# Optimization experiments

Hardware: AMD Instinct MI355X
Metric: run time of the kernel (lower is better)

## Reference

```python
import jax, jax.numpy as jnp
import numpy as np

REFRACTORY_PERIOD = 5
DAMPENING_FACTOR = 0.3


def setup_inputs() -> dict:
    key = jax.random.key(0)
    B, T, N = 32, 4096, 256
    x = jax.random.normal(key, (B, T, N), dtype=jnp.float32)
    return {"x": x}


def _refractory_scan(x):
    # x: [B, T, N]; scan over time keeping refractory counter q resident.
    B, T, N = x.shape
    xt = jnp.swapaxes(x, 0, 1)  # [T, B, N]

    def step(q, x_t):
        cond = (x_t > 0) & (q == 0)
        z_t = jnp.where(cond, jnp.ones_like(q), jnp.zeros_like(q))
        q = jnp.maximum(jnp.zeros_like(q), q - 1) + REFRACTORY_PERIOD * z_t
        return q, z_t

    q0 = jnp.zeros((B, N), dtype=x.dtype)
    # Note: the t=0 case in the original (z0 = x0>0, q = R*z0) is exactly the
    # first step of this scan starting from q0 = 0.
    _, z = jax.lax.scan(step, q0, xt)
    return jnp.swapaxes(z, 0, 1)  # [B, T, N]


def reference(x) -> jnp.ndarray:
    # Forward value is exactly z_forward (the surrogate-gradient straight-through
    # construction leaves the value unchanged).
    return _refractory_scan(x)
```

## Files before the change

kernel.cpp:

```cpp
#include <hip/hip_runtime.h>
#include <cstdint>
#include <cstddef>

#define BB 32
#define TT 4096
#define NNV 64
#define CC 32
#define PSUB 4
#define PG 32
#define NCH 256

__device__ __forceinline__ uint32_t comp6(uint32_t f, uint32_t g) {
    uint32_t h = 0;
    #pragma unroll
    for (int e = 0; e < 6; ++e) {
        const uint32_t fe = (f >> (4 * e)) & 0xFu;
        h |= ((g >> (4 * fe)) & 0xFu) << (4 * e);
    }
    return h;
}

__device__ __forceinline__ uint32_t tbl_from_mask(uint32_t m) {
    uint32_t tbl = 0;
    #pragma unroll
    for (int e = 0; e < 6; ++e) {
        int na = e;
        #pragma unroll
        for (int it = 0; it < 6; ++it) {
            const uint32_t r = (na < 32) ? (m >> na) : 0u;
            const int t = na + (r ? __builtin_ctz(r) : 0);
            na = r ? (t + 6) : na;
        }
        const int q = na > CC ? na - CC : 0;
        tbl |= (uint32_t)q << (4 * e);
    }
    return tbl;
}

__global__ __launch_bounds__(256) void k_scan(const float* __restrict__ x,
                                              uint4* __restrict__ msk,
                                              uint32_t* __restrict__ gtab) {
    const int tid = threadIdx.x;
    const int pg = blockIdx.x >> 5;
    const int b  = blockIdx.x & 31;
    const int psub = tid >> 6;
    const int n4 = tid & 63;
    const int p = pg * PSUB + psub;

    const float4* __restrict__ xv = reinterpret_cast<const float4*>(x)
        + ((size_t)b * TT + (size_t)p * CC) * NNV + n4;

    uint32_t cur[4] = {0u, 0u, 0u, 0u};
    #pragma unroll
    for (int jb = 0; jb < CC; jb += 8) {
        float4 buf[8];
        #pragma unroll
        for (int u = 0; u < 8; ++u)
            buf[u] = xv[(size_t)(jb + u) * NNV];
        #pragma unroll
        for (int u = 0; u < 8; ++u) {
            const int j = jb + u;
            cur[0] |= (buf[u].x > 0.0f) ? (1u << j) : 0u;
            cur[1] |= (buf[u].y > 0.0f) ? (1u << j) : 0u;
            cur[2] |= (buf[u].z > 0.0f) ? (1u << j) : 0u;
            cur[3] |= (buf[u].w > 0.0f) ? (1u << j) : 0u;
        }
    }

    msk[(size_t)blockIdx.x * 256 + tid] = make_uint4(cur[0], cur[1], cur[2], cur[3]);

    __shared__ uint32_t tbl[PSUB][NCH];
    __shared__ uint32_t aux[2][NCH];
    #pragma unroll
    for (int c = 0; c < 4; ++c)
        tbl[psub][n4 * 4 + c] = tbl_from_mask(cur[c]);
    __syncthreads();
    aux[0][tid] = comp6(tbl[0][tid], tbl[1][tid]);
    aux[1][tid] = comp6(tbl[2][tid], tbl[3][tid]);
    __syncthreads();
    gtab[(size_t)blockIdx.x * 256 + tid] = comp6(aux[0][tid], aux[1][tid]);
}

__global__ __launch_bounds__(256) void k_emit(const uint4* __restrict__ msk,
                                              const uint32_t* __restrict__ gtab,
                                              float* __restrict__ z) {
    const int tid = threadIdx.x;
    const int pg = blockIdx.x >> 5;
    const int b  = blockIdx.x & 31;
    const int psub = tid >> 6;
    const int n4 = tid & 63;
    const int p = pg * PSUB + psub;

    __shared__ uint32_t gl[PG - 1][NCH];
    __shared__ uint32_t tbl[PSUB][NCH];
    __shared__ uint8_t  ent[PSUB][NCH];

    for (int i = tid; i < pg * NCH; i += 256)
        gl[0][i] = gtab[((size_t)(i >> 8) * 32 + b) * 256 + (i & 255)];

    const uint4 mv = msk[(size_t)blockIdx.x * 256 + tid];
    uint32_t cur[4] = {mv.x, mv.y, mv.z, mv.w};
    #pragma unroll
    for (int c = 0; c < 4; ++c)
        tbl[psub][n4 * 4 + c] = tbl_from_mask(cur[c]);
    __syncthreads();

    {
        int e = 0;
        for (int g = 0; g < pg; ++g)
            e = (int)((gl[g][tid] >> (4 * e)) & 0xFu);
        #pragma unroll
        for (int s = 0; s < PSUB; ++s) {
            ent[s][tid] = (uint8_t)e;
            e = (int)((tbl[s][tid] >> (4 * e)) & 0xFu);
        }
    }
    __syncthreads();

    float4* __restrict__ zv = reinterpret_cast<float4*>(z)
        + ((size_t)b * TT + (size_t)p * CC) * NNV + n4;

    const uint32_t e4 = reinterpret_cast<const uint32_t*>(ent[psub])[n4];
    uint32_t spk[4];
    #pragma unroll
    for (int c = 0; c < 4; ++c) {
        const uint32_t m = cur[c];
        int na = (int)((e4 >> (8 * c)) & 0xFFu);
        uint32_t s = 0;
        #pragma unroll
        for (int it = 0; it < 6; ++it) {
            const uint32_t r = (na < 32) ? (m >> na) : 0u;
            const int t = na + (r ? __builtin_ctz(r) : 0);
            s |= r ? (1u << (t & 31)) : 0u;
            na = r ? (t + 6) : na;
        }
        spk[c] = s;
    }

    #pragma unroll
    for (int j = 0; j < CC; ++j) {
        float4 o;
        o.x = ((spk[0] >> j) & 1u) ? 1.0f : 0.0f;
        o.y = ((spk[1] >> j) & 1u) ? 1.0f : 0.0f;
        o.z = ((spk[2] >> j) & 1u) ? 1.0f : 0.0f;
        o.w = ((spk[3] >> j) & 1u) ? 1.0f : 0.0f;
        zv[(size_t)j * NNV] = o;
    }
}

extern "C" void kernel_launch(void* const* d_in, const int* in_sizes, int n_in,
                              void* d_out, int out_size, void* d_ws, size_t ws_size,
                              hipStream_t stream) {
    const float* x = (const float*)d_in[0];
    float* z = (float*)d_out;
    uint4* msk = (uint4*)d_ws;
    uint32_t* gtab = (uint32_t*)((char*)d_ws + (size_t)BB * PG * PSUB * NCH * 4);

    k_scan<<<dim3(BB * PG), 256, 0, stream>>>(x, msk, gtab);
    k_emit<<<dim3(BB * PG), 256, 0, stream>>>(msk, gtab, z);
}
```

Measured before the change: 251.4 us.

## Stage scan tables in output buffer, add resolve kernel, use nontemporal stores

```diff
diff --git a/kernel.cpp b/kernel.cpp
--- a/kernel.cpp
+++ b/kernel.cpp
@@ -9,6 +9,16 @@
 #define PSUB 4
 #define PG 32
 #define NCH 256
+#define OFF_MSK 0u
+#define OFF_MAP 4096u
+#define OFF_TBL 5120u
+#define OFF_ENT 9216u
+
+typedef float f32x4 __attribute__((ext_vector_type(4)));
+
+__device__ __forceinline__ char* region_of(float* z, int b, int pg) {
+    return (char*)(z + ((size_t)b * TT + (size_t)pg * (CC * PSUB)) * NCH);
+}
 
 __device__ __forceinline__ uint32_t comp6(uint32_t f, uint32_t g) {
     uint32_t h = 0;
@@ -38,8 +48,7 @@
 }
 
 __global__ __launch_bounds__(256) void k_scan(const float* __restrict__ x,
-                                              uint4* __restrict__ msk,
-                                              uint32_t* __restrict__ gtab) {
+                                              float* __restrict__ z) {
     const int tid = threadIdx.x;
     const int pg = blockIdx.x >> 5;
     const int b  = blockIdx.x & 31;
@@ -67,23 +76,58 @@
         }
     }
 
-    msk[(size_t)blockIdx.x * 256 + tid] = make_uint4(cur[0], cur[1], cur[2], cur[3]);
+    char* regionB = region_of(z, b, pg);
+    reinterpret_cast<uint4*>(regionB + OFF_MSK)[tid] =
+        make_uint4(cur[0], cur[1], cur[2], cur[3]);
 
     __shared__ uint32_t tbl[PSUB][NCH];
     __shared__ uint32_t aux[2][NCH];
+    uint32_t* tblg = reinterpret_cast<uint32_t*>(regionB + OFF_TBL);
     #pragma unroll
-    for (int c = 0; c < 4; ++c)
-        tbl[psub][n4 * 4 + c] = tbl_from_mask(cur[c]);
+    for (int c = 0; c < 4; ++c) {
+        const uint32_t t = tbl_from_mask(cur[c]);
+        tbl[psub][n4 * 4 + c] = t;
+        tblg[psub * NCH + n4 * 4 + c] = t;
+    }
     __syncthreads();
     aux[0][tid] = comp6(tbl[0][tid], tbl[1][tid]);
     aux[1][tid] = comp6(tbl[2][tid], tbl[3][tid]);
     __syncthreads();
-    gtab[(size_t)blockIdx.x * 256 + tid] = comp6(aux[0][tid], aux[1][tid]);
+    reinterpret_cast<uint32_t*>(regionB + OFF_MAP)[tid] =
+        comp6(aux[0][tid], aux[1][tid]);
 }
 
-__global__ __launch_bounds__(256) void k_emit(const uint4* __restrict__ msk,
-                                              const uint32_t* __restrict__ gtab,
-                                              float* __restrict__ z) {
+__global__ __launch_bounds__(256) void k_resolve(float* __restrict__ z) {
+    const int tid = threadIdx.x;
+    const int pg = blockIdx.x >> 5;
+    const int b  = blockIdx.x & 31;
+
+    __shared__ uint32_t gl[PG - 1][NCH];
+    for (int i = tid; i < pg * NCH; i += 256) {
+        const char* rg = region_of(z, b, i >> 8);
+        gl[0][i] = reinterpret_cast<const uint32_t*>(rg + OFF_MAP)[i & 255];
+    }
+
+    char* regionB = region_of(z, b, pg);
+    const uint32_t* tblg = reinterpret_cast<const uint32_t*>(regionB + OFF_TBL);
+    uint32_t t4[PSUB];
+    #pragma unroll
+    for (int s = 0; s < PSUB; ++s) t4[s] = tblg[s * NCH + tid];
+    __syncthreads();
+
+    int e = 0;
+    for (int g = 0; g < pg; ++g)
+        e = (int)((gl[g][tid] >> (4 * e)) & 0xFu);
+
+    uint8_t* ent = reinterpret_cast<uint8_t*>(regionB + OFF_ENT);
+    #pragma unroll
+    for (int s = 0; s < PSUB; ++s) {
+        ent[s * NCH + tid] = (uint8_t)e;
+        e = (int)((t4[s] >> (4 * e)) & 0xFu);
+    }
+}
+
+__global__ __launch_bounds__(256) void k_emit(float* __restrict__ z) {
     const int tid = threadIdx.x;
     const int pg = blockIdx.x >> 5;
     const int b  = blockIdx.x & 31;
@@ -91,36 +135,13 @@
     const int n4 = tid & 63;
     const int p = pg * PSUB + psub;
 
-    __shared__ uint32_t gl[PG - 1][NCH];
-    __shared__ uint32_t tbl[PSUB][NCH];
-    __shared__ uint8_t  ent[PSUB][NCH];
-
-    for (int i = tid; i < pg * NCH; i += 256)
-        gl[0][i] = gtab[((size_t)(i >> 8) * 32 + b) * 256 + (i & 255)];
-
-    const uint4 mv = msk[(size_t)blockIdx.x * 256 + tid];
-    uint32_t cur[4] = {mv.x, mv.y, mv.z, mv.w};
-    #pragma unroll
-    for (int c = 0; c < 4; ++c)
-        tbl[psub][n4 * 4 + c] = tbl_from_mask(cur[c]);
+    char* regionB = region_of(z, b, pg);
+    const uint4 mv = reinterpret_cast<const uint4*>(regionB + OFF_MSK)[tid];
+    const uint32_t e4 = *reinterpret_cast<const uint32_t*>(
+        regionB + OFF_ENT + (size_t)psub * NCH + n4 * 4);
     __syncthreads();
 
-    {
-        int e = 0;
-        for (int g = 0; g < pg; ++g)
-            e = (int)((gl[g][tid] >> (4 * e)) & 0xFu);
-        #pragma unroll
-        for (int s = 0; s < PSUB; ++s) {
-            ent[s][tid] = (uint8_t)e;
-            e = (int)((tbl[s][tid] >> (4 * e)) & 0xFu);
-        }
-    }
-    __syncthreads();
-
-    float4* __restrict__ zv = reinterpret_cast<float4*>(z)
-        + ((size_t)b * TT + (size_t)p * CC) * NNV + n4;
-
-    const uint32_t e4 = reinterpret_cast<const uint32_t*>(ent[psub])[n4];
+    const uint32_t cur[4] = {mv.x, mv.y, mv.z, mv.w};
     uint32_t spk[4];
     #pragma unroll
     for (int c = 0; c < 4; ++c) {
@@ -137,14 +158,16 @@
         spk[c] = s;
     }
 
+    f32x4* __restrict__ zv = reinterpret_cast<f32x4*>(z)
+        + ((size_t)b * TT + (size_t)p * CC) * NNV + n4;
+
     #pragma unroll
     for (int j = 0; j < CC; ++j) {
-        float4 o;
-        o.x = ((spk[0] >> j) & 1u) ? 1.0f : 0.0f;
-        o.y = ((spk[1] >> j) & 1u) ? 1.0f : 0.0f;
-        o.z = ((spk[2] >> j) & 1u) ? 1.0f : 0.0f;
-        o.w = ((spk[3] >> j) & 1u) ? 1.0f : 0.0f;
-        zv[(size_t)j * NNV] = o;
+        f32x4 o = { ((spk[0] >> j) & 1u) ? 1.0f : 0.0f,
+                    ((spk[1] >> j) & 1u) ? 1.0f : 0.0f,
+                    ((spk[2] >> j) & 1u) ? 1.0f : 0.0f,
+                    ((spk[3] >> j) & 1u) ? 1.0f : 0.0f };
+        __builtin_nontemporal_store(o, &zv[(size_t)j * NNV]);
     }
 }
 
@@ -153,9 +176,9 @@
                               hipStream_t stream) {
     const float* x = (const float*)d_in[0];
     float* z = (float*)d_out;
-    uint4* msk = (uint4*)d_ws;
-    uint32_t* gtab = (uint32_t*)((char*)d_ws + (size_t)BB * PG * PSUB * NCH * 4);
+    (void)d_ws; (void)ws_size;
 
-    k_scan<<<dim3(BB * PG), 256, 0, stream>>>(x, msk, gtab);
-    k_emit<<<dim3(BB * PG), 256, 0, stream>>>(msk, gtab, z);
+    k_scan<<<dim3(BB * PG), 256, 0, stream>>>(x, z);
+    k_resolve<<<dim3(BB * PG), 256, 0, stream>>>(z);
+    k_emit<<<dim3(BB * PG), 256, 0, stream>>>(z);
 }
```

New measurement: 262.6 us. 4.5% more time.
